# Kernel tuning notes

Measured on AMD Instinct MI355X. Metric: run time of the kernel, lower is better.

Reference implementation:

```python
import jax, jax.numpy as jnp
import numpy as np

B, S, E = 2, 2048, 2048
A, H = 2048, 16  # attention_dim, n_heads
HD = A // H      # head_dim = 128
ROPE_THETA = 10000.0


def setup_inputs() -> dict:
    key = jax.random.key(0)
    k1, k2, k3 = jax.random.split(key, 3)
    x = jax.random.normal(k1, (B, S, E), dtype=jnp.float32)
    W_qkv = jax.random.normal(k2, (E, 3 * A), dtype=jnp.float32) * 0.02
    W_out = jax.random.normal(k3, (A, E), dtype=jnp.float32) * 0.02
    return {"x": x, "W_qkv": W_qkv, "W_out": W_out}


def _apply_rope(x):
    # x: (B, H, S, D); interleaved rotary pairs (rotary-embedding-torch default)
    b, h, s, d = x.shape
    inv_freq = 1.0 / (ROPE_THETA ** (jnp.arange(0, d, 2, dtype=jnp.float32) / d))
    freqs = jnp.arange(s, dtype=jnp.float32)[:, None] * inv_freq[None, :]  # (S, D/2)
    cos, sin = jnp.cos(freqs), jnp.sin(freqs)
    xr = x.reshape(b, h, s, d // 2, 2)
    x1, x2 = xr[..., 0], xr[..., 1]
    o1 = x1 * cos - x2 * sin
    o2 = x1 * sin + x2 * cos
    return jnp.stack([o1, o2], axis=-1).reshape(b, h, s, d)


def reference(x, W_qkv, W_out):
    b, s, _ = x.shape
    qkv = (x @ W_qkv).reshape(b, s, 3, H, HD)          # (B,S,3,H,hd)
    qkv = jnp.moveaxis(qkv, 3, 1)                      # movedim(-2,1) -> (B,H,S,3,hd)
    q, k, v = qkv[..., 0, :], qkv[..., 1, :], qkv[..., 2, :]
    q = _apply_rope(q)
    k = _apply_rope(k)
    scale = 1.0 / jnp.sqrt(jnp.asarray(HD, dtype=x.dtype))
    scores = jnp.einsum("bhqd,bhkd->bhqk", q, k) * scale
    attn = jax.nn.softmax(scores, axis=-1)
    out = jnp.einsum("bhqk,bhkd->bhqd", attn, v)       # (B,H,S,hd)
    out = out.transpose(0, 2, 1, 3).reshape(b, s, A)   # (B,S,A)
    return out @ W_out
```

## Files before the change

### kernel.cpp

```cpp
#include <hip/hip_runtime.h>
#include <math.h>

typedef float  f32x4  __attribute__((ext_vector_type(4)));
typedef short  s16x8 __attribute__((ext_vector_type(8)));
typedef short  s16x4 __attribute__((ext_vector_type(4)));
typedef unsigned short u16;
typedef unsigned int u32;

static __device__ __forceinline__ u16 f32_to_bf16_rne(float f) {
    u32 u = __builtin_bit_cast(u32, f);
    u32 r = u + 0x7fffu + ((u >> 16) & 1u);
    return (u16)(r >> 16);
}
static __device__ __forceinline__ u32 pack_bf16_rhu(float a, float b) {
    u32 ua = __builtin_bit_cast(u32, a);
    u32 ub = __builtin_bit_cast(u32, b);
    return ((ua + 0x8000u) >> 16) | ((ub + 0x8000u) & 0xffff0000u);
}

static __device__ __forceinline__ void gl2lds16(const void* g, void* l) {
    __builtin_amdgcn_global_load_lds(
        (const __attribute__((address_space(1))) u32*)g,
        (__attribute__((address_space(3))) u32*)l, 16, 0, 0);
}

__global__ __launch_bounds__(256) void k_prep(const float* __restrict__ x,
                                              const float* __restrict__ Wq,
                                              const float* __restrict__ Wo,
                                              u16* __restrict__ xb,
                                              u16* __restrict__ Wqt,
                                              u16* __restrict__ Wot) {
    __shared__ float TT[64 * 130];
    const int blk = blockIdx.x;
    const int t = threadIdx.x;
    if (blk < 4096) {
        int i = (blk * 256 + t) * 8;
        float4 a = *reinterpret_cast<const float4*>(x + i);
        float4 b = *reinterpret_cast<const float4*>(x + i + 4);
        s16x8 o;
        o[0] = (short)f32_to_bf16_rne(a.x); o[1] = (short)f32_to_bf16_rne(a.y);
        o[2] = (short)f32_to_bf16_rne(a.z); o[3] = (short)f32_to_bf16_rne(a.w);
        o[4] = (short)f32_to_bf16_rne(b.x); o[5] = (short)f32_to_bf16_rne(b.y);
        o[6] = (short)f32_to_bf16_rne(b.z); o[7] = (short)f32_to_bf16_rne(b.w);
        *reinterpret_cast<s16x8*>(xb + i) = o;
        return;
    }
    const float* in; u16* out; int C, ct, rt;
    if (blk < 5632) {
        int tb = blk - 4096; ct = tb % 96; rt = tb / 96; in = Wq; out = Wqt; C = 6144;
    } else {
        int tb = blk - 5632; ct = tb % 32; rt = tb / 32; in = Wo; out = Wot; C = 2048;
    }
    const int R = 2048;
    const int tr = t >> 4, tc = t & 15;
    float4 v[8];
#pragma unroll
    for (int u = 0; u < 8; ++u) {
        int r = u * 16 + tr;
        v[u] = *reinterpret_cast<const float4*>(in + (size_t)(rt * 128 + r) * C + ct * 64 + tc * 4);
    }
#pragma unroll
    for (int u = 0; u < 8; ++u) {
        int r = u * 16 + tr;
        TT[(tc * 4 + 0) * 130 + r] = v[u].x;
        TT[(tc * 4 + 1) * 130 + r] = v[u].y;
        TT[(tc * 4 + 2) * 130 + r] = v[u].z;
        TT[(tc * 4 + 3) * 130 + r] = v[u].w;
    }
    __syncthreads();
#pragma unroll
    for (int u = 0; u < 4; ++u) {
        int oc = u * 16 + tr;
        int r0 = tc * 8;
        s16x8 o;
#pragma unroll
        for (int e = 0; e < 8; ++e)
            o[e] = (short)f32_to_bf16_rne(TT[oc * 130 + r0 + e]);
        *reinterpret_cast<s16x8*>(out + (size_t)(ct * 64 + oc) * R + rt * 128 + r0) = o;
    }
}

__global__ __launch_bounds__(512, 2) void k_gemm384(const u16* __restrict__ Amat,
                                                    const u16* __restrict__ Bt,
                                                    u16* __restrict__ Cout,
                                                    u16* __restrict__ Vt,
                                                    int M, int N, int K) {
    __shared__ __align__(16) u16 As[2][128 * 64];
    __shared__ __align__(16) u16 Bs[2][384 * 64];
    const int t = threadIdx.x;
    const int lane = t & 63, wave = t >> 6;
    const int m16 = lane & 15, qd = lane >> 4;
    const int wr = wave >> 2, wc = wave & 3;
    const int srow = lane >> 3;
    const int sch = (lane & 7) ^ srow;

    int bx, by;
    if (gridDim.x == 16 && gridDim.y == 32) {
        int orig = blockIdx.y * gridDim.x + blockIdx.x;
        int xcd = orig & 7, loc = orig >> 3;
        int cx = xcd & 3, cy = xcd >> 2;
        bx = cx * 4 + (loc & 3);
        by = cy * 16 + (loc >> 2);
    } else {
        bx = blockIdx.x; by = blockIdx.y;
    }
    const size_t m0 = (size_t)by * 128, n0 = (size_t)bx * 384;

    const u16* Ab = Amat + m0 * (size_t)K;
    const u16* Bb = Bt + n0 * (size_t)K;
    const int NT = K >> 6;

    auto stage128 = [&](const u16* gbase, u16* lbase, int k0) {
        int rb0 = wave * 8;
        gl2lds16(gbase + (size_t)(rb0 + srow) * K + k0 + sch * 8, lbase + rb0 * 64);
        int rb1 = rb0 + 64;
        gl2lds16(gbase + (size_t)(rb1 + srow) * K + k0 + sch * 8, lbase + rb1 * 64);
    };

    f32x4 acc[4][6] = {};
    s16x8 af[4][2], bq[6][2];

    stage128(Bb,                   &Bs[0][0],        0);
    stage128(Bb + 128 * (size_t)K, &Bs[0][128 * 64], 0);
    stage128(Bb + 256 * (size_t)K, &Bs[0][256 * 64], 0);
    stage128(Ab,                   &As[0][0],        0);
    if (NT > 1) {
        stage128(Bb,                   &Bs[1][0],        64);
        stage128(Bb + 128 * (size_t)K, &Bs[1][128 * 64], 64);
        asm volatile("s_waitcnt vmcnt(4)" ::: "memory");
    } else {
        asm volatile("s_waitcnt vmcnt(0)" ::: "memory");
    }
    __builtin_amdgcn_s_barrier();

    for (int kt = 0; kt < NT; ++kt) {
        const int p = kt & 1;

#pragma unroll
        for (int i = 0; i < 4; ++i) {
            int ra = wr * 64 + i * 16 + m16;
            af[i][0] = *reinterpret_cast<const s16x8*>(&As[p][ra * 64 + ((qd)     ^ (ra & 7)) * 8]);
        }
#pragma unroll
        for (int j = 0; j < 6; ++j) {
            int rb = wc * 96 + j * 16 + m16;
            bq[j][0] = *reinterpret_cast<const s16x8*>(&Bs[p][rb * 64 + ((qd)     ^ (rb & 7)) * 8]);
        }
        if (kt + 1 < NT) stage128(Bb + 256 * (size_t)K, &Bs[p ^ 1][256 * 64], (kt + 1) << 6);
#pragma unroll
        for (int i = 0; i < 4; ++i) {
            int ra = wr * 64 + i * 16 + m16;
            af[i][1] = *reinterpret_cast<const s16x8*>(&As[p][ra * 64 + ((4 + qd) ^ (ra & 7)) * 8]);
        }
#pragma unroll
        for (int j = 0; j < 6; ++j) {
            int rb = wc * 96 + j * 16 + m16;
            bq[j][1] = *reinterpret_cast<const s16x8*>(&Bs[p][rb * 64 + ((4 + qd) ^ (rb & 7)) * 8]);
        }
        if (kt + 1 < NT) stage128(Ab, &As[p ^ 1][0], (kt + 1) << 6);

        __builtin_amdgcn_s_setprio(1);
#pragma unroll
        for (int i = 0; i < 4; ++i)
#pragma unroll
            for (int j = 0; j < 6; ++j)
                acc[i][j] = __builtin_amdgcn_mfma_f32_16x16x32_bf16(af[i][0], bq[j][0], acc[i][j], 0, 0, 0);
        __builtin_amdgcn_s_setprio(0);

        asm volatile("s_waitcnt lgkmcnt(0)" ::: "memory");
        __builtin_amdgcn_s_barrier();

        if (kt + 2 < NT) {
            stage128(Bb,                   &Bs[p][0],        (kt + 2) << 6);
            stage128(Bb + 128 * (size_t)K, &Bs[p][128 * 64], (kt + 2) << 6);
        }
        __builtin_amdgcn_s_setprio(1);
#pragma unroll
        for (int i = 0; i < 4; ++i)
#pragma unroll
            for (int j = 0; j < 6; ++j)
                acc[i][j] = __builtin_amdgcn_mfma_f32_16x16x32_bf16(af[i][1], bq[j][1], acc[i][j], 0, 0, 0);
        __builtin_amdgcn_s_setprio(0);
        if (kt + 2 < NT) {
            asm volatile("s_waitcnt vmcnt(4)" ::: "memory");
        } else {
            asm volatile("s_waitcnt vmcnt(0)" ::: "memory");
        }
        __builtin_amdgcn_s_barrier();
    }

    {
        float invf[6];
#pragma unroll
        for (int j = 0; j < 6; ++j) {
            int pi = ((int)(n0 + wc * 96 + j * 16 + m16) & 127) >> 1;
            invf[j] = __expf(-0.14391156831f * (float)pi);
        }
#pragma unroll
        for (int i = 0; i < 4; ++i)
#pragma unroll
            for (int j = 0; j < 6; ++j) {
                size_t colbase = n0 + wc * 96 + j * 16;
                if (colbase < 4096) {
#pragma unroll
                    for (int r = 0; r < 4; ++r) {
                        float v = acc[i][j][r];
                        float pv = __shfl_xor(v, 1);
                        size_t row = m0 + wr * 64 + i * 16 + qd * 4 + r;
                        float f = (float)(int)(row & 2047) * invf[j];
                        float sn, cs;
                        __sincosf(f, &sn, &cs);
                        float res = (m16 & 1) ? fmaf(pv, sn, v * cs) : fmaf(v, cs, -pv * sn);
                        Cout[row * N + colbase + m16] = f32_to_bf16_rne(res);
                    }
                } else {
                    int vcol = (int)colbase - 4096 + m16;
                    int h = vcol >> 7, d = vcol & 127;
                    size_t row0 = m0 + wr * 64 + i * 16 + qd * 4;
                    int b = (int)(row0 >> 11);
                    int s = (int)(row0 & 2047);
                    s16x4 o;
#pragma unroll
                    for (int r = 0; r < 4; ++r)
                        o[r] = (short)f32_to_bf16_rne(acc[i][j][r]);
                    *reinterpret_cast<s16x4*>(
                        Vt + ((size_t)(b * 16 + h)) * 262144 + (size_t)d * 2048 + s) = o;
                }
            }
    }
}

__global__ __launch_bounds__(512, 2) void k_gemmo(const u16* __restrict__ Amat,
                                                  const u16* __restrict__ Bt,
                                                  float* __restrict__ Cout,
                                                  int M, int N, int K) {
    __shared__ __align__(16) u16 As[2][128 * 64];
    __shared__ __align__(16) u16 Bs[2][256 * 64];
    const int t = threadIdx.x;
    const int lane = t & 63, wave = t >> 6;
    const int m16 = lane & 15, qd = lane >> 4;
    const int wr = wave >> 2, wc = wave & 3;
    const int srow = lane >> 3;
    const int sch = (lane & 7) ^ srow;

    int bx, by;
    if (gridDim.x == 8 && gridDim.y == 32) {
        int orig = blockIdx.y * gridDim.x + blockIdx.x;
        int xcd = orig & 7, loc = orig >> 3;
        int cx = xcd & 1, cy = xcd >> 1;
        bx = cx * 4 + (loc & 3);
        by = cy * 8 + (loc >> 2);
    } else {
        bx = blockIdx.x; by = blockIdx.y;
    }
    const size_t m0 = (size_t)by * 128, n0 = (size_t)bx * 256;

    const u16* Ab = Amat + m0 * (size_t)K;
    const u16* Bb = Bt + n0 * (size_t)K;
    const int NT = K >> 6;

    auto stage128 = [&](const u16* gbase, u16* lbase, int k0) {
        int rb0 = wave * 8;
        gl2lds16(gbase + (size_t)(rb0 + srow) * K + k0 + sch * 8, lbase + rb0 * 64);
        int rb1 = rb0 + 64;
        gl2lds16(gbase + (size_t)(rb1 + srow) * K + k0 + sch * 8, lbase + rb1 * 64);
    };

    f32x4 acc[4][4] = {};
    s16x8 af[4][2], bq[4][2];

    stage128(Ab,                   &As[0][0],        0);
    stage128(Bb,                   &Bs[0][0],        0);
    stage128(Bb + 128 * (size_t)K, &Bs[0][128 * 64], 0);
    if (NT > 1) {
        stage128(Ab,               &As[1][0],        64);
        stage128(Bb,               &Bs[1][0],        64);
        asm volatile("s_waitcnt vmcnt(4)" ::: "memory");
    } else {
        asm volatile("s_waitcnt vmcnt(0)" ::: "memory");
    }
    __builtin_amdgcn_s_barrier();

    for (int kt = 0; kt < NT; ++kt) {
        const int p = kt & 1;

#pragma unroll
        for (int i = 0; i < 4; ++i) {
            int ra = wr * 64 + i * 16 + m16;
            af[i][0] = *reinterpret_cast<const s16x8*>(&As[p][ra * 64 + ((qd)     ^ (ra & 7)) * 8]);
        }
#pragma unroll
        for (int j = 0; j < 4; ++j) {
            int rb = wc * 64 + j * 16 + m16;
            bq[j][0] = *reinterpret_cast<const s16x8*>(&Bs[p][rb * 64 + ((qd)     ^ (rb & 7)) * 8]);
        }
        if (kt + 1 < NT) stage128(Bb + 128 * (size_t)K, &Bs[p ^ 1][128 * 64], (kt + 1) << 6);
#pragma unroll
        for (int i = 0; i < 4; ++i) {
            int ra = wr * 64 + i * 16 + m16;
            af[i][1] = *reinterpret_cast<const s16x8*>(&As[p][ra * 64 + ((4 + qd) ^ (ra & 7)) * 8]);
        }
#pragma unroll
        for (int j = 0; j < 4; ++j) {
            int rb = wc * 64 + j * 16 + m16;
            bq[j][1] = *reinterpret_cast<const s16x8*>(&Bs[p][rb * 64 + ((4 + qd) ^ (rb & 7)) * 8]);
        }

        __builtin_amdgcn_s_setprio(1);
#pragma unroll
        for (int i = 0; i < 4; ++i)
#pragma unroll
            for (int j = 0; j < 4; ++j)
                acc[i][j] = __builtin_amdgcn_mfma_f32_16x16x32_bf16(af[i][0], bq[j][0], acc[i][j], 0, 0, 0);
        __builtin_amdgcn_s_setprio(0);

        asm volatile("s_waitcnt lgkmcnt(0)" ::: "memory");
        __builtin_amdgcn_s_barrier();

        if (kt + 2 < NT) {
            stage128(Ab, &As[p][0], (kt + 2) << 6);
            stage128(Bb, &Bs[p][0], (kt + 2) << 6);
        }
        __builtin_amdgcn_s_setprio(1);
#pragma unroll
        for (int i = 0; i < 4; ++i)
#pragma unroll
            for (int j = 0; j < 4; ++j)
                acc[i][j] = __builtin_amdgcn_mfma_f32_16x16x32_bf16(af[i][1], bq[j][1], acc[i][j], 0, 0, 0);
        __builtin_amdgcn_s_setprio(0);
        if (kt + 2 < NT) {
            asm volatile("s_waitcnt vmcnt(4)" ::: "memory");
        } else {
            asm volatile("s_waitcnt vmcnt(0)" ::: "memory");
        }
        __builtin_amdgcn_s_barrier();
    }

#pragma unroll
    for (int i = 0; i < 4; ++i)
#pragma unroll
        for (int j = 0; j < 4; ++j)
#pragma unroll
            for (int r = 0; r < 4; ++r) {
                size_t row = m0 + wr * 64 + i * 16 + qd * 4 + r;
                size_t col = n0 + wc * 64 + j * 16 + m16;
                Cout[row * N + col] = acc[i][j][r];
            }
}

__global__ __launch_bounds__(512, 4) void k_flash(const u16* __restrict__ qkv,
                                                  const u16* __restrict__ vt,
                                                  u16* __restrict__ out) {
    __shared__ __align__(16) u16 KS[128 * 136];
    __shared__ __align__(16) u16 VS[128 * 136];
    const int t = threadIdx.x, lane = t & 63, wave = t >> 6;
    const int m16 = lane & 15, qd = lane >> 4;
    const int bh = blockIdx.y, b = bh >> 4, h = bh & 15;
    const int q0 = blockIdx.x * 128;
    const u16* Qg = qkv + (size_t)b * 2048 * 6144 + (size_t)h * 128;
    const u16* Kg = Qg + 2048;
    const u16* Vtg = vt + (size_t)bh * 128 * 2048;
    const float C2 = 0.12751743f;

    int srow[4], scol[4], pi0[4];
#pragma unroll
    for (int ci = 0; ci < 4; ++ci) {
        int idx = ci * 512 + t;
        int row = idx >> 4, c = idx & 15;
        srow[ci] = row;
        scol[ci] = c * 8;
        pi0[ci] = 32 * (c >> 2) + 16 * (c & 1) + 4 * ((c >> 1) & 1);
    }

    s16x8 qf[4];
#pragma unroll
    for (int kc = 0; kc < 4; ++kc)
        qf[kc] = *reinterpret_cast<const s16x8*>(
            Qg + (size_t)(q0 + wave * 16 + m16) * 6144 + kc * 32 + qd * 8);

    f32x4 accO[8] = {};
    float mrow = -1e30f, lrow = 0.f;

    for (int kt = 0; kt < 16; ++kt) {
        const int s0 = kt * 128;
        s16x8 kreg[4], vreg[4];
#pragma unroll
        for (int ci = 0; ci < 4; ++ci) {
            kreg[ci] = *reinterpret_cast<const s16x8*>(
                Kg + (size_t)(s0 + srow[ci]) * 6144 + scol[ci]);
            vreg[ci] = *reinterpret_cast<const s16x8*>(
                Vtg + (size_t)srow[ci] * 2048 + s0 + scol[ci]);
        }
        __syncthreads();
#pragma unroll
        for (int ci = 0; ci < 4; ++ci) {
            *reinterpret_cast<s16x8*>(&KS[srow[ci] * 136 + scol[ci]]) = kreg[ci];
            s16x4 lo = __builtin_shufflevector(vreg[ci], vreg[ci], 0, 1, 2, 3);
            s16x4 hi = __builtin_shufflevector(vreg[ci], vreg[ci], 4, 5, 6, 7);
            *reinterpret_cast<s16x4*>(&VS[srow[ci] * 136 + pi0[ci]]) = lo;
            *reinterpret_cast<s16x4*>(&VS[srow[ci] * 136 + pi0[ci] + 8]) = hi;
        }
        __syncthreads();

        f32x4 accS[8] = {};
#pragma unroll
        for (int kc = 0; kc < 4; ++kc)
#pragma unroll
            for (int nj = 0; nj < 8; ++nj) {
                s16x8 kf = *reinterpret_cast<const s16x8*>(
                    &KS[(nj * 16 + m16) * 136 + (kc * 4 + qd) * 8]);
                accS[nj] = __builtin_amdgcn_mfma_f32_16x16x32_bf16(kf, qf[kc], accS[nj], 0, 0, 0);
            }

        float mx = accS[0][0];
#pragma unroll
        for (int nj = 0; nj < 8; ++nj)
#pragma unroll
            for (int r = 0; r < 4; ++r) mx = fmaxf(mx, accS[nj][r]);
        mx *= C2;
        mx = fmaxf(mx, __shfl_xor(mx, 16));
        mx = fmaxf(mx, __shfl_xor(mx, 32));
        float mn = fmaxf(mrow, mx);
        float alpha = __builtin_amdgcn_exp2f(mrow - mn);
        mrow = mn;
        float ls = 0.f;
        s16x4 pk[8];
#pragma unroll
        for (int nj = 0; nj < 8; ++nj) {
            float p0 = __builtin_amdgcn_exp2f(fmaf(accS[nj][0], C2, -mn));
            float p1 = __builtin_amdgcn_exp2f(fmaf(accS[nj][1], C2, -mn));
            float p2 = __builtin_amdgcn_exp2f(fmaf(accS[nj][2], C2, -mn));
            float p3 = __builtin_amdgcn_exp2f(fmaf(accS[nj][3], C2, -mn));
            ls += (p0 + p1) + (p2 + p3);
            u32 lo = pack_bf16_rhu(p0, p1);
            u32 hi = pack_bf16_rhu(p2, p3);
            uint2 pr = make_uint2(lo, hi);
            pk[nj] = __builtin_bit_cast(s16x4, pr);
        }
        ls += __shfl_xor(ls, 16);
        ls += __shfl_xor(ls, 32);
        lrow = lrow * alpha + ls;
        float aO[4];
#pragma unroll
        for (int r = 0; r < 4; ++r) aO[r] = __shfl(alpha, qd * 4 + r);
#pragma unroll
        for (int dj = 0; dj < 8; ++dj)
#pragma unroll
            for (int r = 0; r < 4; ++r) accO[dj][r] *= aO[r];

#pragma unroll
        for (int kb = 0; kb < 4; ++kb) {
            s16x8 af = __builtin_shufflevector(pk[2 * kb], pk[2 * kb + 1],
                                               0, 1, 2, 3, 4, 5, 6, 7);
#pragma unroll
            for (int dj = 0; dj < 8; ++dj) {
                s16x8 vf = *reinterpret_cast<const s16x8*>(
                    &VS[(dj * 16 + m16) * 136 + kb * 32 + qd * 8]);
                accO[dj] = __builtin_amdgcn_mfma_f32_16x16x32_bf16(af, vf, accO[dj], 0, 0, 0);
            }
        }
    }
    float invl = 1.0f / lrow;
    float iv[4];
#pragma unroll
    for (int r = 0; r < 4; ++r) iv[r] = __shfl(invl, qd * 4 + r);
#pragma unroll
    for (int r = 0; r < 4; ++r) {
        size_t row = (size_t)b * 2048 + q0 + wave * 16 + qd * 4 + r;
#pragma unroll
        for (int dj = 0; dj < 8; ++dj)
            out[row * 2048 + h * 128 + dj * 16 + m16] =
                f32_to_bf16_rne(accO[dj][r] * iv[r]);
    }
}

extern "C" void kernel_launch(void* const* d_in, const int* in_sizes, int n_in,
                              void* d_out, int out_size, void* d_ws, size_t ws_size,
                              hipStream_t stream) {
    const float* x     = (const float*)d_in[0];
    const float* W_qkv = (const float*)d_in[1];
    const float* W_out = (const float*)d_in[2];
    float* out = (float*)d_out;

    char* ws = (char*)d_ws;
    u16* xb   = (u16*)(ws);
    u16* Wqt  = (u16*)(ws + (16u << 20));
    u16* Wot  = (u16*)(ws + (40u << 20));
    u16* qkvb = (u16*)(ws + (48u << 20));
    u16* attn = (u16*)(ws + (96u << 20));
    u16* vtg  = (u16*)(ws + (112u << 20));

    k_prep<<<6144, 256, 0, stream>>>(x, W_qkv, W_out, xb, Wqt, Wot);
    k_gemm384<<<dim3(16, 32), 512, 0, stream>>>(xb, Wqt, qkvb, vtg, 4096, 6144, 2048);
    k_flash<<<dim3(16, 32), 512, 0, stream>>>(qkvb, vtg, attn);
    k_gemmo<<<dim3(8, 32), 512, 0, stream>>>(attn, Wot, out, 4096, 2048, 2048);
}
```

Before: 390.5 us.

## Permute QKV weight columns per head and stage V transpose through LDS

The prep kernel reorders the QKV weight columns so that each 384-wide GEMM tile holds 256 Q/K columns and the 128 V columns of one head. The QKV GEMM epilogue then writes transposed V into shared memory first and emits coalesced 16-byte global stores, replacing scattered 8-byte stores. This aims to cut the uncoalesced V-transpose write traffic. It adds an LDS round trip and a barrier, and the row stride of 130 leaves the vector LDS accesses only partially aligned.

```diff
diff --git a/kernel.cpp b/kernel.cpp
--- a/kernel.cpp
+++ b/kernel.cpp
@@ -23,6 +23,7 @@
         (const __attribute__((address_space(1))) u32*)g,
         (__attribute__((address_space(3))) u32*)l, 16, 0, 0);
 }
+
 
 __global__ __launch_bounds__(256) void k_prep(const float* __restrict__ x,
                                               const float* __restrict__ Wq,
@@ -45,11 +46,11 @@
         *reinterpret_cast<s16x8*>(xb + i) = o;
         return;
     }
-    const float* in; u16* out; int C, ct, rt;
+    const float* in; u16* out; int C, ct, rt; bool perm;
     if (blk < 5632) {
-        int tb = blk - 4096; ct = tb % 96; rt = tb / 96; in = Wq; out = Wqt; C = 6144;
+        int tb = blk - 4096; ct = tb % 96; rt = tb / 96; in = Wq; out = Wqt; C = 6144; perm = true;
     } else {
-        int tb = blk - 5632; ct = tb % 32; rt = tb / 32; in = Wo; out = Wot; C = 2048;
+        int tb = blk - 5632; ct = tb % 32; rt = tb / 32; in = Wo; out = Wot; C = 2048; perm = false;
     }
     const int R = 2048;
     const int tr = t >> 4, tc = t & 15;
@@ -76,7 +77,13 @@
 #pragma unroll
         for (int e = 0; e < 8; ++e)
             o[e] = (short)f32_to_bf16_rne(TT[oc * 130 + r0 + e]);
-        *reinterpret_cast<s16x8*>(out + (size_t)(ct * 64 + oc) * R + rt * 128 + r0) = o;
+        int n = ct * 64 + oc;
+        int nn = n;
+        if (perm) {
+            if (n < 4096) nn = (n >> 8) * 384 + (n & 255);
+            else { int vv = n - 4096; nn = (vv >> 7) * 384 + 256 + (vv & 127); }
+        }
+        *reinterpret_cast<s16x8*>(out + (size_t)nn * R + rt * 128 + r0) = o;
     }
 }
 
@@ -85,8 +92,8 @@
                                                     u16* __restrict__ Cout,
                                                     u16* __restrict__ Vt,
                                                     int M, int N, int K) {
-    __shared__ __align__(16) u16 As[2][128 * 64];
-    __shared__ __align__(16) u16 Bs[2][384 * 64];
+    __shared__ __align__(16) u16 SMEM[2 * 128 * 64 + 2 * 384 * 64];
+    const int AS_SZ = 128 * 64, BS_SZ = 384 * 64;
     const int t = threadIdx.x;
     const int lane = t & 63, wave = t >> 6;
     const int m16 = lane & 15, qd = lane >> 4;
@@ -120,44 +127,53 @@
     f32x4 acc[4][6] = {};
     s16x8 af[4][2], bq[6][2];
 
-    stage128(Bb,                   &Bs[0][0],        0);
-    stage128(Bb + 128 * (size_t)K, &Bs[0][128 * 64], 0);
-    stage128(Bb + 256 * (size_t)K, &Bs[0][256 * 64], 0);
-    stage128(Ab,                   &As[0][0],        0);
-    if (NT > 1) {
-        stage128(Bb,                   &Bs[1][0],        64);
-        stage128(Bb + 128 * (size_t)K, &Bs[1][128 * 64], 64);
-        asm volatile("s_waitcnt vmcnt(4)" ::: "memory");
-    } else {
-        asm volatile("s_waitcnt vmcnt(0)" ::: "memory");
+    {
+        u16* A0 = SMEM;
+        u16* B0 = SMEM + 2 * AS_SZ;
+        stage128(Bb,                   B0,            0);
+        stage128(Bb + 128 * (size_t)K, B0 + 128 * 64, 0);
+        stage128(Bb + 256 * (size_t)K, B0 + 256 * 64, 0);
+        stage128(Ab,                   A0,            0);
+        if (NT > 1) {
+            u16* B1 = B0 + BS_SZ;
+            stage128(Bb,                   B1,            64);
+            stage128(Bb + 128 * (size_t)K, B1 + 128 * 64, 64);
+            asm volatile("s_waitcnt vmcnt(4)" ::: "memory");
+        } else {
+            asm volatile("s_waitcnt vmcnt(0)" ::: "memory");
+        }
     }
     __builtin_amdgcn_s_barrier();
 
     for (int kt = 0; kt < NT; ++kt) {
         const int p = kt & 1;
+        u16* Ap  = SMEM + p * AS_SZ;
+        u16* Bp  = SMEM + 2 * AS_SZ + p * BS_SZ;
+        u16* Anx = SMEM + (p ^ 1) * AS_SZ;
+        u16* Bnx = SMEM + 2 * AS_SZ + (p ^ 1) * BS_SZ;
 
 #pragma unroll
         for (int i = 0; i < 4; ++i) {
             int ra = wr * 64 + i * 16 + m16;
-            af[i][0] = *reinterpret_cast<const s16x8*>(&As[p][ra * 64 + ((qd)     ^ (ra & 7)) * 8]);
+            af[i][0] = *reinterpret_cast<const s16x8*>(&Ap[ra * 64 + ((qd)     ^ (ra & 7)) * 8]);
         }
 #pragma unroll
         for (int j = 0; j < 6; ++j) {
             int rb = wc * 96 + j * 16 + m16;
-            bq[j][0] = *reinterpret_cast<const s16x8*>(&Bs[p][rb * 64 + ((qd)     ^ (rb & 7)) * 8]);
-        }
-        if (kt + 1 < NT) stage128(Bb + 256 * (size_t)K, &Bs[p ^ 1][256 * 64], (kt + 1) << 6);
+            bq[j][0] = *reinterpret_cast<const s16x8*>(&Bp[rb * 64 + ((qd)     ^ (rb & 7)) * 8]);
+        }
+        if (kt + 1 < NT) stage128(Bb + 256 * (size_t)K, Bnx + 256 * 64, (kt + 1) << 6);
 #pragma unroll
         for (int i = 0; i < 4; ++i) {
             int ra = wr * 64 + i * 16 + m16;
-            af[i][1] = *reinterpret_cast<const s16x8*>(&As[p][ra * 64 + ((4 + qd) ^ (ra & 7)) * 8]);
+            af[i][1] = *reinterpret_cast<const s16x8*>(&Ap[ra * 64 + ((4 + qd) ^ (ra & 7)) * 8]);
         }
 #pragma unroll
         for (int j = 0; j < 6; ++j) {
             int rb = wc * 96 + j * 16 + m16;
-            bq[j][1] = *reinterpret_cast<const s16x8*>(&Bs[p][rb * 64 + ((4 + qd) ^ (rb & 7)) * 8]);
-        }
-        if (kt + 1 < NT) stage128(Ab, &As[p ^ 1][0], (kt + 1) << 6);
+            bq[j][1] = *reinterpret_cast<const s16x8*>(&Bp[rb * 64 + ((4 + qd) ^ (rb & 7)) * 8]);
+        }
+        if (kt + 1 < NT) stage128(Ab, Anx, (kt + 1) << 6);
 
         __builtin_amdgcn_s_setprio(1);
 #pragma unroll
@@ -171,8 +187,8 @@
         __builtin_amdgcn_s_barrier();
 
         if (kt + 2 < NT) {
-            stage128(Bb,                   &Bs[p][0],        (kt + 2) << 6);
-            stage128(Bb + 128 * (size_t)K, &Bs[p][128 * 64], (kt + 2) << 6);
+            stage128(Bb,                   Bp,            (kt + 2) << 6);
+            stage128(Bb + 128 * (size_t)K, Bp + 128 * 64, (kt + 2) << 6);
         }
         __builtin_amdgcn_s_setprio(1);
 #pragma unroll
@@ -190,18 +206,23 @@
     }
 
     {
+        u16* VS = SMEM;
         float invf[6];
 #pragma unroll
         for (int j = 0; j < 6; ++j) {
-            int pi = ((int)(n0 + wc * 96 + j * 16 + m16) & 127) >> 1;
-            invf[j] = __expf(-0.14391156831f * (float)pi);
+            int lc = wc * 96 + j * 16;
+            if (lc < 256) {
+                int oc = bx * 256 + lc + m16;
+                invf[j] = __expf(-0.14391156831f * (float)((oc & 127) >> 1));
+            } else invf[j] = 0.f;
         }
 #pragma unroll
         for (int i = 0; i < 4; ++i)
 #pragma unroll
             for (int j = 0; j < 6; ++j) {
-                size_t colbase = n0 + wc * 96 + j * 16;
-                if (colbase < 4096) {
+                int lc = wc * 96 + j * 16;
+                if (lc < 256) {
+                    int oc = bx * 256 + lc + m16;
 #pragma unroll
                     for (int r = 0; r < 4; ++r) {
                         float v = acc[i][j][r];
@@ -211,22 +232,29 @@
                         float sn, cs;
                         __sincosf(f, &sn, &cs);
                         float res = (m16 & 1) ? fmaf(pv, sn, v * cs) : fmaf(v, cs, -pv * sn);
-                        Cout[row * N + colbase + m16] = f32_to_bf16_rne(res);
+                        Cout[row * N + oc] = f32_to_bf16_rne(res);
                     }
                 } else {
-                    int vcol = (int)colbase - 4096 + m16;
-                    int h = vcol >> 7, d = vcol & 127;
-                    size_t row0 = m0 + wr * 64 + i * 16 + qd * 4;
-                    int b = (int)(row0 >> 11);
-                    int s = (int)(row0 & 2047);
+                    int d = lc - 256 + m16;
+                    int sl = wr * 64 + i * 16 + qd * 4;
                     s16x4 o;
 #pragma unroll
                     for (int r = 0; r < 4; ++r)
                         o[r] = (short)f32_to_bf16_rne(acc[i][j][r]);
-                    *reinterpret_cast<s16x4*>(
-                        Vt + ((size_t)(b * 16 + h)) * 262144 + (size_t)d * 2048 + s) = o;
+                    *reinterpret_cast<s16x4*>(&VS[d * 130 + sl]) = o;
                 }
             }
+        __syncthreads();
+        int b = (int)(m0 >> 11);
+        int sbase = (int)(m0 & 2047);
+        u16* vdst = Vt + ((size_t)(b * 16 + bx)) * 262144;
+        int d = t >> 2, sc = t & 3;
+#pragma unroll
+        for (int e = 0; e < 4; ++e) {
+            int s = sc * 8 + e * 32;
+            s16x8 o = *reinterpret_cast<const s16x8*>(&VS[d * 130 + s]);
+            *reinterpret_cast<s16x8*>(vdst + (size_t)d * 2048 + sbase + s) = o;
+        }
     }
 }
 
```

Result: no change. 396.8 us (+1.6%).
